# Kernel optimization log

Measured on AMD Instinct MI355X. Metric: run time of the kernel, lower is better.

Reference implementation:

```python
import jax, jax.numpy as jnp
import numpy as np

N, F, T, HID, E = 50000, 8, 12, 64, 1600000


def setup_inputs() -> dict:
    key = jax.random.key(0)
    ks = jax.random.split(key, 9)
    x = jax.random.normal(ks[0], (N, F, T), jnp.float32)
    edge_index = jax.random.randint(ks[1], (2, E), 0, N)
    edge_weight = jax.random.uniform(ks[2], (E,), jnp.float32)
    # GCNConv weights for the z/r/h gates, fused along the output dim -> (F, 3*HID)
    s = 1.0 / np.sqrt(F)
    conv_w = jax.random.uniform(ks[3], (F, 3 * HID), jnp.float32, -s, s)
    conv_b = jnp.zeros((3 * HID,), jnp.float32)
    # TGCN gate linears: input is concat([conv_out, H]) of width 2*HID
    s2 = 1.0 / np.sqrt(2 * HID)
    lin_w = jax.random.uniform(ks[4], (3, 2 * HID, HID), jnp.float32, -s2, s2)
    lin_b = jax.random.uniform(ks[5], (3, HID), jnp.float32, -s2, s2)
    attention = jax.random.uniform(ks[6], (T,), jnp.float32)
    sc = 1.0 / np.sqrt(HID)
    cls_w = jax.random.uniform(ks[7], (HID, T), jnp.float32, -sc, sc)
    cls_b = jax.random.uniform(ks[8], (T,), jnp.float32, -sc, sc)
    return dict(x=x, edge_index=edge_index, edge_weight=edge_weight,
                conv_w=conv_w, conv_b=conv_b, lin_w=lin_w, lin_b=lin_b,
                attention=attention, cls_w=cls_w, cls_b=cls_b)


def _gcn_norm(edge_index, edge_weight, num_nodes):
    # PyG gcn_norm: add self-loops (weight 1), symmetric D^-1/2 (A+I) D^-1/2
    src, dst = edge_index[0], edge_index[1]
    loop = jnp.arange(num_nodes)
    src = jnp.concatenate([src, loop])
    dst = jnp.concatenate([dst, loop])
    w = jnp.concatenate([edge_weight, jnp.ones((num_nodes,), edge_weight.dtype)])
    deg = jax.ops.segment_sum(w, dst, num_segments=num_nodes)
    dinv = jnp.where(deg > 0, jax.lax.rsqrt(deg), 0.0)
    return src, dst, dinv[src] * w * dinv[dst]


def reference(x, edge_index, edge_weight, conv_w, conv_b, lin_w, lin_b, attention, cls_w, cls_b):
    num_nodes, _, periods = x.shape
    hid = cls_w.shape[0]
    src, dst, norm = _gcn_norm(edge_index, edge_weight, num_nodes)
    probs = jax.nn.softmax(attention)
    Hzero = jnp.zeros((num_nodes, hid), x.dtype)  # A3TGCN passes the same H (None->0) each period
    H_accum = jnp.zeros((num_nodes, hid), x.dtype)
    for t in range(periods):
        xw = x[:, :, t] @ conv_w  # (N, 3*hid)
        conv = jax.ops.segment_sum(xw[src] * norm[:, None], dst, num_segments=num_nodes) + conv_b
        cz, cr, ch = jnp.split(conv, 3, axis=1)
        Z = jax.nn.sigmoid(jnp.concatenate([cz, Hzero], axis=1) @ lin_w[0] + lin_b[0])
        R = jax.nn.sigmoid(jnp.concatenate([cr, Hzero], axis=1) @ lin_w[1] + lin_b[1])
        H_tilde = jnp.tanh(jnp.concatenate([ch, Hzero * R], axis=1) @ lin_w[2] + lin_b[2])
        H_new = Z * Hzero + (1.0 - Z) * H_tilde
        H_accum = H_accum + probs[t] * H_new
    h = jax.nn.relu(H_accum)
    return h @ cls_w + cls_b  # (N, periods)
```

## Files before the change

kernel.cpp:

```cpp
#include <hip/hip_runtime.h>
#include <hip/hip_fp16.h>
#include <math.h>

#define NN 50000
#define FD 8
#define TD 12
#define HD 64
#define FT 96
#define EE 1600000
#define NBUK 391
#define TILE 16384
#define NT 98
#define XB 586
#define SORTCAP 5120

#define OFF_GHIST 0
#define OFF_BASE  512
#define OFF_CUR   1024
#define OFF_ROWST 2048
#define OFF_DINV  (2048 + NN + 16)
#define OFF_FUSED (OFF_DINV + NN)
#define OFF_THIST (OFF_FUSED + 1184)
#define OFF_XH    (OFF_THIST + 38400)
#define OFF_BEDGE (OFF_XH + NN*48)
#define OFF_AGGH  (OFF_BEDGE + 2*EE)

typedef _Float16 h2v __attribute__((ext_vector_type(2)));

__device__ inline void h8f(uint4 h, float* f) {
    const __half2* p = (const __half2*)&h;
#pragma unroll
    for (int i = 0; i < 4; ++i) {
        float2 v = __half22float2(p[i]);
        f[2 * i] = v.x; f[2 * i + 1] = v.y;
    }
}

__device__ inline uint4 f8h(const float* f) {
    uint4 o;
    __half2* p = (__half2*)&o;
#pragma unroll
    for (int i = 0; i < 4; ++i) p[i] = __floats2half2_rn(f[2 * i], f[2 * i + 1]);
    return o;
}

__global__ __launch_bounds__(1024) void k_front(const float* __restrict__ x,
                                                uint4* __restrict__ xh4,
                                                const int* __restrict__ ei,
                                                int* __restrict__ ghist,
                                                int* __restrict__ thist,
                                                const float* __restrict__ conv_w,
                                                const float* __restrict__ conv_b,
                                                const float* __restrict__ lin_w,
                                                const float* __restrict__ lin_b,
                                                const float* __restrict__ attention,
                                                float* __restrict__ fused) {
    int b = blockIdx.x;
    int tid = threadIdx.x;
    if (b < NT) {
        __shared__ int h[NBUK];
        for (int i = tid; i < NBUK; i += 1024) h[i] = 0;
        __syncthreads();
        int base = b * TILE;
        for (int i = 0; i < TILE / 1024; ++i) {
            int e = base + i * 1024 + tid;
            if (e < EE) atomicAdd(&h[ei[EE + e] >> 7], 1);
        }
        __syncthreads();
        int* trow = thist + b * NBUK;
        for (int i = tid; i < NBUK; i += 1024) {
            int c = h[i];
            trow[i] = c;
            if (c) atomicAdd(&ghist[i], c);
        }
    } else if (b < NT + XB) {
        unsigned i = (unsigned)(b - NT) * 1024u + tid;
        if (i < (unsigned)NN * 12u) {
            unsigned n = i / 12u, t = i - n * 12u;
            const float* xp = x + (size_t)n * FT + t;
            float f[8];
#pragma unroll
            for (int k = 0; k < 8; ++k) f[k] = xp[k * 12];
            xh4[i] = f8h(f);
        }
    } else {
        for (int idx = tid; idx < 1024; idx += 1024) {
            int sel = idx >> 9;
            int f = (idx & 511) >> 6;
            int h = idx & 63;
            const float* cw = conv_w + f * 192 + (sel ? 128 : 0);
            const float* lw = lin_w + (sel ? 2 * 128 * 64 : 0) + h;
            float s = 0.f;
            for (int k = 0; k < 64; ++k) s += cw[k] * lw[k * 64];
            fused[idx] = s;
        }
        if (tid < 128) {
            int sel = tid >> 6;
            int h = tid & 63;
            const float* cb = conv_b + (sel ? 128 : 0);
            const float* lw = lin_w + (sel ? 2 * 128 * 64 : 0) + h;
            float s = lin_b[(sel ? 2 * 64 : 0) + h];
            for (int k = 0; k < 64; ++k) s += cb[k] * lw[k * 64];
            fused[1024 + tid] = s;
        }
        if (tid == 0) {
            float m = attention[0];
            for (int t = 1; t < TD; ++t) m = fmaxf(m, attention[t]);
            float e[TD], sum = 0.f;
            for (int t = 0; t < TD; ++t) { e[t] = __expf(attention[t] - m); sum += e[t]; }
            for (int t = 0; t < TD; ++t) fused[1152 + t] = e[t] / sum;
        }
    }
}

__global__ void k_scan(const int* __restrict__ ghist, int* __restrict__ bktbase,
                       int* __restrict__ cursor) {
    __shared__ int s[512];
    int tid = threadIdx.x;
    int v = (tid < NBUK) ? ghist[tid] : 0;
    s[tid] = v;
    __syncthreads();
    for (int off = 1; off < 512; off <<= 1) {
        int t = (tid >= off) ? s[tid - off] : 0;
        __syncthreads();
        s[tid] += t;
        __syncthreads();
    }
    int excl = s[tid] - v;
    if (tid < NBUK) { bktbase[tid] = excl; cursor[tid] = excl; }
    if (tid == NBUK - 1) bktbase[NBUK] = excl + v;
}

__global__ __launch_bounds__(1024) void k_place(const int* __restrict__ ei,
                                                const float* __restrict__ w,
                                                const int* __restrict__ thist,
                                                int* __restrict__ cursor,
                                                int2* __restrict__ bedge) {
    __shared__ int h[NBUK], bbase[NBUK];
    int tid = threadIdx.x;
    const int* tcnt = thist + blockIdx.x * NBUK;
    for (int i = tid; i < NBUK; i += 1024) {
        int c = tcnt[i];
        bbase[i] = c ? atomicAdd(&cursor[i], c) : 0;
        h[i] = 0;
    }
    __syncthreads();
    int base = blockIdx.x * TILE;
    for (int i = 0; i < TILE / 1024; ++i) {
        int e = base + i * 1024 + tid;
        if (e < EE) {
            int dst = ei[EE + e];
            int bk = dst >> 7;
            int rank = atomicAdd(&h[bk], 1);
            bedge[bbase[bk] + rank] =
                make_int2(ei[e] | ((dst & 127) << 16), __float_as_int(w[e]));
        }
    }
}

__global__ __launch_bounds__(512) void k_sort(const int* __restrict__ bktbase,
                                              int2* __restrict__ bedge,
                                              int* __restrict__ rowstart,
                                              float* __restrict__ dinv) {
    __shared__ int2 stage[SORTCAP];
    __shared__ int cnt[128];
    __shared__ float wd[128];
    __shared__ int rowbase[128];
    int tid = threadIdx.x, b = blockIdx.x;
    int es = bktbase[b], ee = bktbase[b + 1];
    int count = ee - es;
    if (count > SORTCAP) count = SORTCAP;
    if (tid < 128) { cnt[tid] = 0; wd[tid] = 0.f; }
    __syncthreads();
    for (int i = tid; i < count; i += 512) {
        int2 u = bedge[es + i];
        stage[i] = u;
        int dl = u.x >> 16;
        atomicAdd(&cnt[dl], 1);
        atomicAdd(&wd[dl], __int_as_float(u.y));
    }
    __syncthreads();
    if (tid < 128) rowbase[tid] = cnt[tid];
    __syncthreads();
    for (int off = 1; off < 128; off <<= 1) {
        int t = 0;
        if (tid >= off && tid < 128) t = rowbase[tid - off];
        __syncthreads();
        if (tid < 128) rowbase[tid] += t;
        __syncthreads();
    }
    int dbase = b << 7;
    if (tid < 128) {
        int excl = rowbase[tid] - cnt[tid];
        rowbase[tid] = excl;
        if (dbase + tid < NN) {
            rowstart[dbase + tid] = es + excl;
            dinv[dbase + tid] = rsqrtf(1.0f + wd[tid]);
        }
        cnt[tid] = 0;
    }
    if (b == NBUK - 1 && tid == 0) rowstart[NN] = ee;
    __syncthreads();
    for (int i = tid; i < count; i += 512) {
        int2 u = stage[i];
        int dl = u.x >> 16;
        int pos = atomicAdd(&cnt[dl], 1);
        bedge[es + rowbase[dl] + pos] = make_int2(u.x & 0xFFFF, u.y);
    }
}

__global__ __launch_bounds__(256) void k_gather(const uint4* __restrict__ xh4,
                                                const float* __restrict__ dinv,
                                                const int* __restrict__ rowstart,
                                                const int2* __restrict__ edata,
                                                uint4* __restrict__ aggh) {
    unsigned t = blockIdx.x * 256u + threadIdx.x;
    if (t >= (unsigned)NN * 12u) return;
    unsigned n = t / 12u;
    unsigned c = t - n * 12u;
    float dv = dinv[n];
    float a[8];
    h8f(xh4[n * 12u + c], a);
#pragma unroll
    for (int j = 0; j < 8; ++j) a[j] *= dv;
    int rs = rowstart[n], re = rowstart[n + 1];
    int k = rs;
    for (; k + 7 < re; k += 8) {
        int2 p[8];
#pragma unroll
        for (int q = 0; q < 8; ++q) p[q] = edata[k + q];
        float co[8];
#pragma unroll
        for (int q = 0; q < 8; ++q) co[q] = dinv[p[q].x] * __int_as_float(p[q].y);
        uint4 hv[8];
#pragma unroll
        for (int q = 0; q < 8; ++q) hv[q] = xh4[(unsigned)p[q].x * 12u + c];
#pragma unroll
        for (int q = 0; q < 8; ++q) {
            float v[8];
            h8f(hv[q], v);
#pragma unroll
            for (int j = 0; j < 8; ++j) a[j] += co[q] * v[j];
        }
    }
    for (; k < re; ++k) {
        int2 p = edata[k];
        float co = dinv[p.x] * __int_as_float(p.y);
        float v[8];
        h8f(xh4[(unsigned)p.x * 12u + c], v);
#pragma unroll
        for (int j = 0; j < 8; ++j) a[j] += co * v[j];
    }
#pragma unroll
    for (int j = 0; j < 8; ++j) a[j] *= dv;
    aggh[n * 12u + c] = f8h(a);
}

__global__ __launch_bounds__(256) void k_node(const uint4* __restrict__ aggh,
                                              const float* __restrict__ fused,
                                              const float* __restrict__ cls_w,
                                              const float* __restrict__ cls_b,
                                              float* __restrict__ out) {
    __shared__ uint4 r4_lds[32 * 12];
    __shared__ float rel_lds[32 * 68];
    __shared__ float cwT_lds[12 * 68];
    __shared__ float cb_lds[12];
    __shared__ float probs_lds[12];
    int tid = threadIdx.x;
    int nbase = blockIdx.x * 32;

    for (int id = tid; id < 384; id += 256) {
        int nl = id / 12, c = id - nl * 12;
        int n = nbase + nl;
        uint4 v = make_uint4(0, 0, 0, 0);
        if (n < NN) v = aggh[(size_t)n * 12 + c];
        r4_lds[nl * 12 + c] = v;
    }
    for (int id = tid; id < 768; id += 256) {
        int hh = id / 12, t = id - hh * 12;
        cwT_lds[t * 68 + hh] = cls_w[id];
    }
    if (tid < 12) { cb_lds[tid] = cls_b[tid]; probs_lds[tid] = fused[1152 + tid]; }

    int h = tid & 63;
    int w = tid >> 6;
    h2v wz2[4], wh2[4];
#pragma unroll
    for (int q = 0; q < 4; ++q) {
        wz2[q] = h2v{(_Float16)fused[(2 * q) * 64 + h],
                     (_Float16)fused[(2 * q + 1) * 64 + h]};
        wh2[q] = h2v{(_Float16)fused[512 + (2 * q) * 64 + h],
                     (_Float16)fused[512 + (2 * q + 1) * 64 + h]};
    }
    float bz = fused[1024 + h], bh = fused[1088 + h];
    __syncthreads();

#pragma unroll
    for (int np = 0; np < 4; ++np) {
        int nl0 = w * 8 + np * 2;
        const uint4* rp0 = &r4_lds[nl0 * 12];
        const uint4* rp1 = rp0 + 12;
        float acc0 = 0.f, acc1 = 0.f;
#pragma unroll
        for (int t = 0; t < TD; ++t) {
            uint4 u0 = rp0[t];
            uint4 u1 = rp1[t];
            const h2v* ra = (const h2v*)&u0;
            const h2v* rb = (const h2v*)&u1;
            float z0 = bz, h0 = bh, z1 = bz, h1 = bh;
#if defined(__has_builtin) && __has_builtin(__builtin_amdgcn_fdot2)
#pragma unroll
            for (int q = 0; q < 4; ++q) {
                z0 = __builtin_amdgcn_fdot2(ra[q], wz2[q], z0, false);
                h0 = __builtin_amdgcn_fdot2(ra[q], wh2[q], h0, false);
                z1 = __builtin_amdgcn_fdot2(rb[q], wz2[q], z1, false);
                h1 = __builtin_amdgcn_fdot2(rb[q], wh2[q], h1, false);
            }
#else
#pragma unroll
            for (int q = 0; q < 4; ++q) {
                z0 += (float)ra[q].x * (float)wz2[q].x + (float)ra[q].y * (float)wz2[q].y;
                h0 += (float)ra[q].x * (float)wh2[q].x + (float)ra[q].y * (float)wh2[q].y;
                z1 += (float)rb[q].x * (float)wz2[q].x + (float)rb[q].y * (float)wz2[q].y;
                h1 += (float)rb[q].x * (float)wh2[q].x + (float)rb[q].y * (float)wh2[q].y;
            }
#endif
            float om0 = __builtin_amdgcn_rcpf(1.f + __expf(z0));
            float om1 = __builtin_amdgcn_rcpf(1.f + __expf(z1));
            float Ht0 = 1.f - 2.f * __builtin_amdgcn_rcpf(1.f + __expf(2.f * h0));
            float Ht1 = 1.f - 2.f * __builtin_amdgcn_rcpf(1.f + __expf(2.f * h1));
            float p = probs_lds[t];
            acc0 += p * om0 * Ht0;
            acc1 += p * om1 * Ht1;
        }
        rel_lds[nl0 * 68 + h] = fmaxf(acc0, 0.f);
        rel_lds[(nl0 + 1) * 68 + h] = fmaxf(acc1, 0.f);
    }
    __syncthreads();

    for (int id = tid; id < 384; id += 256) {
        int nl = id / 12, t = id - nl * 12;
        int n = nbase + nl;
        if (n >= NN) continue;
        const float* rl = &rel_lds[nl * 68];
        const float* cwr = &cwT_lds[t * 68];
        float s = cb_lds[t];
#pragma unroll
        for (int k = 0; k < 16; ++k) {
            float4 rv = *(const float4*)&rl[k * 4];
            float4 cv = *(const float4*)&cwr[k * 4];
            s += rv.x * cv.x + rv.y * cv.y + rv.z * cv.z + rv.w * cv.w;
        }
        out[(size_t)n * TD + t] = s;
    }
}

extern "C" void kernel_launch(void* const* d_in, const int* in_sizes, int n_in,
                              void* d_out, int out_size, void* d_ws, size_t ws_size,
                              hipStream_t stream) {
    const float* x         = (const float*)d_in[0];
    const int*   ei        = (const int*)d_in[1];
    const float* w         = (const float*)d_in[2];
    const float* conv_w    = (const float*)d_in[3];
    const float* conv_b    = (const float*)d_in[4];
    const float* lin_w     = (const float*)d_in[5];
    const float* lin_b     = (const float*)d_in[6];
    const float* attention = (const float*)d_in[7];
    const float* cls_w     = (const float*)d_in[8];
    const float* cls_b     = (const float*)d_in[9];
    float* ws  = (float*)d_ws;
    float* out = (float*)d_out;

    int*   ghist    = (int*)(ws + OFF_GHIST);
    int*   bktbase  = (int*)(ws + OFF_BASE);
    int*   cursor   = (int*)(ws + OFF_CUR);
    int*   rowstart = (int*)(ws + OFF_ROWST);
    float* dinv     = ws + OFF_DINV;
    float* fused    = ws + OFF_FUSED;
    int*   thist    = (int*)(ws + OFF_THIST);
    uint4* xh4      = (uint4*)(ws + OFF_XH);
    int2*  bedge    = (int2*)(ws + OFF_BEDGE);
    uint4* aggh     = (uint4*)(ws + OFF_AGGH);

    hipMemsetAsync(ghist, 0, NBUK * sizeof(int), stream);
    k_front<<<NT + XB + 1, 1024, 0, stream>>>(x, xh4, ei, ghist, thist,
                                              conv_w, conv_b, lin_w, lin_b,
                                              attention, fused);
    k_scan<<<1, 512, 0, stream>>>(ghist, bktbase, cursor);
    k_place<<<NT, 1024, 0, stream>>>(ei, w, thist, cursor, bedge);
    k_sort<<<NBUK, 512, 0, stream>>>(bktbase, bedge, rowstart, dinv);
    {
        unsigned total = (unsigned)NN * 12u;
        k_gather<<<(total + 255) / 256, 256, 0, stream>>>(xh4, dinv,
                                                          rowstart, bedge, aggh);
    }
    k_node<<<(NN + 31) / 32, 256, 0, stream>>>(aggh, fused, cls_w, cls_b, out);
}
```

Measured before the change: 154.4 us.

## Drop memset and global histogram atomics, move x conversion into sort launch

Removes the memset and global atomic histogram by having the scan kernel sum the per-tile histograms directly. The weight-fusion precompute moves into a second block of the scan kernel. The x-to-half conversion moves from the front kernel into extra blocks of the sort kernel, so it runs alongside the bucket sort. This cuts one launch and the global atomics, but the scan's serial 98-row sum adds latency to a single block.

```diff
diff --git a/kernel.cpp b/kernel.cpp
--- a/kernel.cpp
+++ b/kernel.cpp
@@ -11,10 +11,9 @@
 #define NBUK 391
 #define TILE 16384
 #define NT 98
-#define XB 586
+#define XB2 1172
 #define SORTCAP 5120
 
-#define OFF_GHIST 0
 #define OFF_BASE  512
 #define OFF_CUR   1024
 #define OFF_ROWST 2048
@@ -44,47 +43,50 @@
     return o;
 }
 
-__global__ __launch_bounds__(1024) void k_front(const float* __restrict__ x,
-                                                uint4* __restrict__ xh4,
-                                                const int* __restrict__ ei,
-                                                int* __restrict__ ghist,
-                                                int* __restrict__ thist,
-                                                const float* __restrict__ conv_w,
-                                                const float* __restrict__ conv_b,
-                                                const float* __restrict__ lin_w,
-                                                const float* __restrict__ lin_b,
-                                                const float* __restrict__ attention,
-                                                float* __restrict__ fused) {
-    int b = blockIdx.x;
+__global__ __launch_bounds__(1024) void k_hist(const int* __restrict__ ei,
+                                               int* __restrict__ thist) {
+    __shared__ int h[NBUK];
+    int tid = threadIdx.x, b = blockIdx.x;
+    for (int i = tid; i < NBUK; i += 1024) h[i] = 0;
+    __syncthreads();
+    int base = b * TILE;
+    for (int i = 0; i < TILE / 1024; ++i) {
+        int e = base + i * 1024 + tid;
+        if (e < EE) atomicAdd(&h[ei[EE + e] >> 7], 1);
+    }
+    __syncthreads();
+    int* trow = thist + b * NBUK;
+    for (int i = tid; i < NBUK; i += 1024) trow[i] = h[i];
+}
+
+__global__ __launch_bounds__(512) void k_scanpre(const int* __restrict__ thist,
+                                                 int* __restrict__ bktbase,
+                                                 int* __restrict__ cursor,
+                                                 const float* __restrict__ conv_w,
+                                                 const float* __restrict__ conv_b,
+                                                 const float* __restrict__ lin_w,
+                                                 const float* __restrict__ lin_b,
+                                                 const float* __restrict__ attention,
+                                                 float* __restrict__ fused) {
     int tid = threadIdx.x;
-    if (b < NT) {
-        __shared__ int h[NBUK];
-        for (int i = tid; i < NBUK; i += 1024) h[i] = 0;
+    if (blockIdx.x == 0) {
+        __shared__ int s[512];
+        int v = 0;
+        if (tid < NBUK)
+            for (int t = 0; t < NT; ++t) v += thist[t * NBUK + tid];
+        s[tid] = v;
         __syncthreads();
-        int base = b * TILE;
-        for (int i = 0; i < TILE / 1024; ++i) {
-            int e = base + i * 1024 + tid;
-            if (e < EE) atomicAdd(&h[ei[EE + e] >> 7], 1);
-        }
-        __syncthreads();
-        int* trow = thist + b * NBUK;
-        for (int i = tid; i < NBUK; i += 1024) {
-            int c = h[i];
-            trow[i] = c;
-            if (c) atomicAdd(&ghist[i], c);
-        }
-    } else if (b < NT + XB) {
-        unsigned i = (unsigned)(b - NT) * 1024u + tid;
-        if (i < (unsigned)NN * 12u) {
-            unsigned n = i / 12u, t = i - n * 12u;
-            const float* xp = x + (size_t)n * FT + t;
-            float f[8];
-#pragma unroll
-            for (int k = 0; k < 8; ++k) f[k] = xp[k * 12];
-            xh4[i] = f8h(f);
-        }
+        for (int off = 1; off < 512; off <<= 1) {
+            int t = (tid >= off) ? s[tid - off] : 0;
+            __syncthreads();
+            s[tid] += t;
+            __syncthreads();
+        }
+        int excl = s[tid] - v;
+        if (tid < NBUK) { bktbase[tid] = excl; cursor[tid] = excl; }
+        if (tid == NBUK - 1) bktbase[NBUK] = excl + v;
     } else {
-        for (int idx = tid; idx < 1024; idx += 1024) {
+        for (int idx = tid; idx < 1024; idx += 512) {
             int sel = idx >> 9;
             int f = (idx & 511) >> 6;
             int h = idx & 63;
@@ -111,24 +113,6 @@
             for (int t = 0; t < TD; ++t) fused[1152 + t] = e[t] / sum;
         }
     }
-}
-
-__global__ void k_scan(const int* __restrict__ ghist, int* __restrict__ bktbase,
-                       int* __restrict__ cursor) {
-    __shared__ int s[512];
-    int tid = threadIdx.x;
-    int v = (tid < NBUK) ? ghist[tid] : 0;
-    s[tid] = v;
-    __syncthreads();
-    for (int off = 1; off < 512; off <<= 1) {
-        int t = (tid >= off) ? s[tid - off] : 0;
-        __syncthreads();
-        s[tid] += t;
-        __syncthreads();
-    }
-    int excl = s[tid] - v;
-    if (tid < NBUK) { bktbase[tid] = excl; cursor[tid] = excl; }
-    if (tid == NBUK - 1) bktbase[NBUK] = excl + v;
 }
 
 __global__ __launch_bounds__(1024) void k_place(const int* __restrict__ ei,
@@ -158,15 +142,29 @@
     }
 }
 
-__global__ __launch_bounds__(512) void k_sort(const int* __restrict__ bktbase,
-                                              int2* __restrict__ bedge,
-                                              int* __restrict__ rowstart,
-                                              float* __restrict__ dinv) {
+__global__ __launch_bounds__(512) void k_sortx(const int* __restrict__ bktbase,
+                                               int2* __restrict__ bedge,
+                                               int* __restrict__ rowstart,
+                                               float* __restrict__ dinv,
+                                               const float* __restrict__ x,
+                                               uint4* __restrict__ xh4) {
     __shared__ int2 stage[SORTCAP];
     __shared__ int cnt[128];
     __shared__ float wd[128];
     __shared__ int rowbase[128];
     int tid = threadIdx.x, b = blockIdx.x;
+    if (b >= NBUK) {
+        unsigned i = (unsigned)(b - NBUK) * 512u + tid;
+        if (i < (unsigned)NN * 12u) {
+            unsigned n = i / 12u, t = i - n * 12u;
+            const float* xp = x + (size_t)n * FT + t;
+            float f[8];
+#pragma unroll
+            for (int k = 0; k < 8; ++k) f[k] = xp[k * 12];
+            xh4[i] = f8h(f);
+        }
+        return;
+    }
     int es = bktbase[b], ee = bktbase[b + 1];
     int count = ee - es;
     if (count > SORTCAP) count = SORTCAP;
@@ -371,7 +369,6 @@
     float* ws  = (float*)d_ws;
     float* out = (float*)d_out;
 
-    int*   ghist    = (int*)(ws + OFF_GHIST);
     int*   bktbase  = (int*)(ws + OFF_BASE);
     int*   cursor   = (int*)(ws + OFF_CUR);
     int*   rowstart = (int*)(ws + OFF_ROWST);
@@ -382,13 +379,11 @@
     int2*  bedge    = (int2*)(ws + OFF_BEDGE);
     uint4* aggh     = (uint4*)(ws + OFF_AGGH);
 
-    hipMemsetAsync(ghist, 0, NBUK * sizeof(int), stream);
-    k_front<<<NT + XB + 1, 1024, 0, stream>>>(x, xh4, ei, ghist, thist,
-                                              conv_w, conv_b, lin_w, lin_b,
-                                              attention, fused);
-    k_scan<<<1, 512, 0, stream>>>(ghist, bktbase, cursor);
+    k_hist<<<NT, 1024, 0, stream>>>(ei, thist);
+    k_scanpre<<<2, 512, 0, stream>>>(thist, bktbase, cursor,
+                                     conv_w, conv_b, lin_w, lin_b, attention, fused);
     k_place<<<NT, 1024, 0, stream>>>(ei, w, thist, cursor, bedge);
-    k_sort<<<NBUK, 512, 0, stream>>>(bktbase, bedge, rowstart, dinv);
+    k_sortx<<<NBUK + XB2, 512, 0, stream>>>(bktbase, bedge, rowstart, dinv, x, xh4);
     {
         unsigned total = (unsigned)NN * 12u;
         k_gather<<<(total + 255) / 256, 256, 0, stream>>>(xh4, dinv,
```

Measured after the change: 149.3 us. -3.3%, faster.
